# Kernel optimization log

Measured on AMD Instinct MI355X. Metric: run time of the kernel, lower is better.

## Reference

```python
import math
import jax, jax.numpy as jnp
import numpy as np
from jax import lax

B, T, C = 2, 4096, 2048
N_HEAD, N_KV, D = 16, 4, 128
WINDOW, DILATION, CHUNK = 256, 1, 128


def make_rope_cache(seq_len, n_elem, base=10000.0):
    theta = 1.0 / base ** (jnp.arange(0, n_elem, 2, dtype=jnp.float32) / n_elem)
    idx_theta = jnp.arange(seq_len, dtype=jnp.float32)[:, None] * theta[None, :]
    return jnp.stack([jnp.cos(idx_theta), jnp.sin(idx_theta)], axis=-1)  # [T, n_elem/2, 2]


def setup_inputs() -> dict:
    key = jax.random.key(0)
    ks = jax.random.split(key, 5)
    s = 1.0 / math.sqrt(C)
    return {
        "x": jax.random.normal(ks[0], (B, T, C), dtype=jnp.float32),
        "wq": jax.random.normal(ks[1], (N_HEAD * D, C), dtype=jnp.float32) * s,
        "wk": jax.random.normal(ks[2], (N_KV * D, C), dtype=jnp.float32) * s,
        "wv": jax.random.normal(ks[3], (N_KV * D, C), dtype=jnp.float32) * s,
        "wo": jax.random.normal(ks[4], (N_HEAD * D, C), dtype=jnp.float32).T * s,  # stored [out,in]
        "rope_cache": make_rope_cache(T, D),
    }


def apply_rope(xh, cache):
    # xh: [B, T, H, D]; cache: [T, D/2, 2]
    b, t, h, d = xh.shape
    xr = xh.reshape(b, t, h, d // 2, 2)
    cos = cache[:t, :, 0][None, :, None, :]
    sin = cache[:t, :, 1][None, :, None, :]
    x0, x1 = xr[..., 0], xr[..., 1]
    rot = jnp.stack([x0 * cos - x1 * sin, x0 * sin + x1 * cos], axis=-1)
    return rot.reshape(b, t, h, d)


def sliding_attention(q, k, v, window, dilation, chunk):
    # q,k,v: [B, H, T, D] -> [B, H, T, D]; O(T*window), memory bounded via scan over chunks
    b, h, t, d = q.shape
    w = min(window, (t + dilation - 1) // dilation)
    offsets = jnp.arange(w) * dilation
    scale = 1.0 / math.sqrt(d)
    n_chunks = t // chunk

    def step(carry, c):
        pos = c * chunk + jnp.arange(chunk)                       # [L]
        idx_raw = (pos - (w - 1) * dilation)[:, None] + offsets[None, :]  # [L, w]
        invalid = idx_raw < 0
        idx = jnp.clip(idx_raw, 0, t - 1)
        flat = idx.reshape(-1)
        k_win = jnp.take(k, flat, axis=2).reshape(b, h, chunk, w, d)
        v_win = jnp.take(v, flat, axis=2).reshape(b, h, chunk, w, d)
        q_c = lax.dynamic_slice_in_dim(q, c * chunk, chunk, axis=2)
        scores = jnp.einsum('bhld,bhlwd->bhlw', q_c.astype(jnp.float32),
                            k_win.astype(jnp.float32)) * scale
        scores = jnp.where(invalid[None, None], -jnp.inf, scores)
        attn = jax.nn.softmax(scores, axis=-1)
        out_c = jnp.einsum('bhlw,bhlwd->bhld', attn, v_win.astype(jnp.float32))
        return carry, out_c.astype(q.dtype)

    _, outs = lax.scan(step, None, jnp.arange(n_chunks))  # [n_chunks, B, H, chunk, D]
    return outs.transpose(1, 2, 0, 3, 4).reshape(b, h, t, d)


def reference(x, wq, wk, wv, wo, rope_cache):
    b, t, c = x.shape
    q = (x @ wq.T).reshape(b, t, N_HEAD, D)
    k = (x @ wk.T).reshape(b, t, N_KV, D)
    v = (x @ wv.T).reshape(b, t, N_KV, D)
    q = apply_rope(q, rope_cache)
    k = apply_rope(k, rope_cache)
    q = q.transpose(0, 2, 1, 3)  # [B, H, T, D]
    k = k.transpose(0, 2, 1, 3)
    v = v.transpose(0, 2, 1, 3)
    g = N_HEAD // N_KV
    k = jnp.repeat(k, g, axis=1)
    v = jnp.repeat(v, g, axis=1)
    y = sliding_attention(q, k, v, WINDOW, DILATION, CHUNK)
    y = y.transpose(0, 2, 1, 3).reshape(b, t, c)
    return y @ wo.T
```

## Files before the change

### kernel.cpp

```cpp
#include <hip/hip_runtime.h>
#include <stdint.h>

typedef unsigned short u16;
typedef __attribute__((ext_vector_type(8))) short bf16x8;
typedef __attribute__((ext_vector_type(8))) unsigned short u16x8;
typedef __attribute__((ext_vector_type(4))) float f32x4;

#define B_  2
#define T_  4096
#define C_  2048
#define NH  16
#define NKV 4
#define HD  128

__device__ __forceinline__ u16 f2bf(float f) {
  union { float f; uint32_t u; } v; v.f = f;
  uint32_t u = v.u;
  u += 0x7fffu + ((u >> 16) & 1u);
  return (u16)(u >> 16);
}
__device__ __forceinline__ float bf2f(u16 h) {
  union { uint32_t u; float f; } v; v.u = ((uint32_t)h) << 16;
  return v.f;
}

__device__ __forceinline__ void gload_lds16(const u16* g, u16* l) {
  __builtin_amdgcn_global_load_lds(
      (const __attribute__((address_space(1))) void*)g,
      (__attribute__((address_space(3))) void*)l, 16, 0, 0);
}

__global__ void cvt_all(const float* __restrict__ x, const float* __restrict__ wq,
                        const float* __restrict__ wk, const float* __restrict__ wv,
                        const float* __restrict__ wo, u16* __restrict__ xb,
                        u16* __restrict__ wqkv, u16* __restrict__ wob) {
  long i = ((long)blockIdx.x * 256 + threadIdx.x) * 4;
  const float* src; u16* dst; long off;
  if (i < 16777216L)      { src = x;  dst = xb;              off = i; }
  else if (i < 20971520L) { src = wq; dst = wqkv;            off = i - 16777216L; }
  else if (i < 22020096L) { src = wk; dst = wqkv + 4194304L; off = i - 20971520L; }
  else if (i < 23068672L) { src = wv; dst = wqkv + 5242880L; off = i - 22020096L; }
  else                    { src = wo; dst = wob;             off = i - 23068672L; }
  float4 v = *(const float4*)(src + off);
  ushort4 o4;
  o4.x = f2bf(v.x); o4.y = f2bf(v.y); o4.z = f2bf(v.z); o4.w = f2bf(v.w);
  *(ushort4*)(dst + off) = o4;
}

__global__ void krearr(const u16* __restrict__ qkv, u16* __restrict__ K2) {
  int gid = blockIdx.x * 256 + threadIdx.x;
  int r = gid & 65535, bk = gid >> 16;
  int l16 = r & 15, q4 = (r >> 4) & 3, ks = (r >> 6) & 3, kb = r >> 8;
  int bb = bk >> 2, kv = bk & 3;
  const u16* src = qkv + ((long)(bb * T_ + kb * 16 + l16)) * 3072 + 2048 + kv * HD +
                   ks * 32 + q4 * 8;
  *(u16x8*)(K2 + (long)bk * 524288 + (long)r * 8) = *(const u16x8*)src;
}

__global__ __launch_bounds__(256) void vrearr2(const u16* __restrict__ qkv,
                                               u16* __restrict__ V2) {
  const int bid = blockIdx.x;
  const int bk = bid >> 5, kc = bid & 31;
  const int bb = bk >> 2, kv = bk & 3;
  const int t = threadIdx.x;
  __shared__ u16 L[128 * 136];
  {
    int key = t >> 1;
    int dh = (t & 1) * 64;
    const u16* src = qkv + ((long)(bb * T_ + kc * 128 + key)) * 3072 + 2560 + kv * HD + dh;
    u16* dst = L + key * 136 + dh;
#pragma unroll
    for (int u = 0; u < 8; u++)
      *(u16x8*)(dst + u * 8) = *(const u16x8*)(src + u * 8);
  }
  __syncthreads();
  u16* out = V2 + (long)bk * 524288 + (long)kc * 16384;
#pragma unroll
  for (int step = 0; step < 8; step++) {
    int o = step * 256 + t;
    int l16 = o & 15, q4 = (o >> 4) & 3, ks = (o >> 6) & 3, jd = (o >> 8) & 7;
    int keyb = ks * 32 + q4 * 8;
    int d = jd * 16 + l16;
    u16x8 v;
#pragma unroll
    for (int e = 0; e < 8; e++) v[e] = L[(keyb + e) * 136 + d];
    *(u16x8*)(out + (long)o * 8) = v;
  }
}

#define GBAR() __builtin_amdgcn_s_barrier()
#define LGKM0() do { asm volatile("s_waitcnt lgkmcnt(0)" ::: "memory"); \
                     __builtin_amdgcn_sched_barrier(0); } while (0)

template <int WRITE_BF16, int ROPE>
__global__ __launch_bounds__(512, 2) void gemm256(const u16* __restrict__ A,
                                                  const u16* __restrict__ Bw,
                                                  void* __restrict__ Cv,
                                                  const float* __restrict__ rope,
                                                  int M, int N, int K) {
  __shared__ __align__(16) u16 lds[65536];
  const int tid = threadIdx.x;
  const int lane = tid & 63;
  const int wave = tid >> 6;
  const int q4 = lane >> 4, l16 = lane & 15;
  const int wm = wave >> 2, wn = wave & 3;

  const int nwg = gridDim.x * gridDim.y;
  const int orig = blockIdx.y * gridDim.x + blockIdx.x;
  const int swz = (orig & 7) * (nwg >> 3) + (orig >> 3);
  const int bm = swz / gridDim.x, bn = swz % gridDim.x;
  const long m0 = (long)bm * 256, n0 = (long)bn * 256;

  const int srow = tid >> 2;
  const int slot = tid & 3;
  const int sx = (slot ^ ((srow >> 1) & 3)) * 8;
  const u16* Ag0 = A + (m0 + srow) * K + sx;
  const u16* Ag1 = A + (m0 + srow + 128) * K + sx;
  const u16* Bg0 = Bw + (n0 + srow) * K + sx;
  const u16* Bg1 = Bw + (n0 + srow + 128) * K + sx;
  u16* ldst = lds + tid * 8;

  const int nkt = K >> 6;

#define STAGE_A(bufi, kh, kt)                                  \
  do {                                                         \
    long ko = ((long)(kt) << 6) + ((kh) << 5);                 \
    u16* d = ldst + (bufi) * 32768 + (kh) * 8192;              \
    gload_lds16(Ag0 + ko, d);                                  \
    gload_lds16(Ag1 + ko, d + 4096);                           \
  } while (0)
#define STAGE_B(bufi, kh, kt)                                  \
  do {                                                         \
    long ko = ((long)(kt) << 6) + ((kh) << 5);                 \
    u16* d = ldst + (bufi) * 32768 + 16384 + (kh) * 8192;      \
    gload_lds16(Bg0 + ko, d);                                  \
    gload_lds16(Bg1 + ko, d + 4096);                           \
  } while (0)

  int offA[8], offB[4];
#pragma unroll
  for (int m = 0; m < 8; m++) {
    int r = wm * 128 + m * 16 + l16;
    offA[m] = r * 32 + ((q4 ^ ((r >> 1) & 3)) << 3);
  }
#pragma unroll
  for (int n = 0; n < 4; n++) {
    int r = wn * 64 + n * 16 + l16;
    offB[n] = 16384 + r * 32 + ((q4 ^ ((r >> 1) & 3)) << 3);
  }

  f32x4 acc[8][4] = {};

  STAGE_A(0, 0, 0); STAGE_B(0, 0, 0); STAGE_A(0, 1, 0); STAGE_B(0, 1, 0);
  if (nkt > 1) {
    STAGE_A(1, 0, 1); STAGE_B(1, 0, 1);
    asm volatile("s_waitcnt vmcnt(4)" ::: "memory");
  } else {
    asm volatile("s_waitcnt vmcnt(0)" ::: "memory");
  }
  GBAR();

  bf16x8 afX[4], afY[4], bvA[4], bvB[4];
  for (int kt = 0; kt < nkt; kt++) {
    const int bo = (kt & 1) * 32768;
#pragma unroll
    for (int m = 0; m < 4; m++) afX[m] = *(const bf16x8*)(lds + bo + offA[m]);
#pragma unroll
    for (int n = 0; n < 4; n++) bvA[n] = *(const bf16x8*)(lds + bo + offB[n]);
    if (kt + 1 < nkt) STAGE_A((kt + 1) & 1, 1, kt + 1);
    LGKM0();
#pragma unroll
    for (int m = 0; m < 4; m++) afY[m] = *(const bf16x8*)(lds + bo + offA[4 + m]);
    __builtin_amdgcn_s_setprio(1);
#pragma unroll
    for (int m = 0; m < 4; m++)
#pragma unroll
      for (int n = 0; n < 4; n++)
        acc[m][n] = __builtin_amdgcn_mfma_f32_16x16x32_bf16(afX[m], bvA[n], acc[m][n], 0, 0, 0);
    __builtin_amdgcn_s_setprio(0);
    if (kt + 1 < nkt) STAGE_B((kt + 1) & 1, 1, kt + 1);
    LGKM0();
#pragma unroll
    for (int m = 0; m < 4; m++) afX[m] = *(const bf16x8*)(lds + bo + 8192 + offA[m]);
#pragma unroll
    for (int n = 0; n < 4; n++) bvB[n] = *(const bf16x8*)(lds + bo + 8192 + offB[n]);
    __builtin_amdgcn_s_setprio(1);
#pragma unroll
    for (int m = 0; m < 4; m++)
#pragma unroll
      for (int n = 0; n < 4; n++)
        acc[4 + m][n] = __builtin_amdgcn_mfma_f32_16x16x32_bf16(afY[m], bvA[n], acc[4 + m][n], 0, 0, 0);
    __builtin_amdgcn_s_setprio(0);
    GBAR();
    if (kt + 2 < nkt) STAGE_A(kt & 1, 0, kt + 2);
    LGKM0();
#pragma unroll
    for (int m = 0; m < 4; m++) afY[m] = *(const bf16x8*)(lds + bo + 8192 + offA[4 + m]);
    __builtin_amdgcn_s_setprio(1);
#pragma unroll
    for (int m = 0; m < 4; m++)
#pragma unroll
      for (int n = 0; n < 4; n++)
        acc[m][n] = __builtin_amdgcn_mfma_f32_16x16x32_bf16(afX[m], bvB[n], acc[m][n], 0, 0, 0);
    __builtin_amdgcn_s_setprio(0);
    if (kt + 2 < nkt) STAGE_B(kt & 1, 0, kt + 2);
    LGKM0();
    __builtin_amdgcn_s_setprio(1);
#pragma unroll
    for (int m = 0; m < 4; m++)
#pragma unroll
      for (int n = 0; n < 4; n++)
        acc[4 + m][n] = __builtin_amdgcn_mfma_f32_16x16x32_bf16(afY[m], bvB[n], acc[4 + m][n], 0, 0, 0);
    __builtin_amdgcn_s_setprio(0);
    if (kt + 2 < nkt)
      asm volatile("s_waitcnt vmcnt(4)" ::: "memory");
    else
      asm volatile("s_waitcnt vmcnt(0)" ::: "memory");
    GBAR();
  }
#undef STAGE_A
#undef STAGE_B

  if (ROPE) {
    float* rl = (float*)lds;
    const int rrow = tid >> 1;
    const int rh = (tid & 1) * 64;
    const int rx = ((rrow >> 2) & 3) << 3;
    const float* rsrc = rope + ((long)((int)((m0 + rrow)) & (T_ - 1)) * 128 + rh);
    float* rdst = rl + rrow * 128;
#pragma unroll
    for (int v = 0; v < 16; v++) {
      int col = rh + v * 4;
      *(float4*)(rdst + (col ^ rx)) = *(const float4*)(rsrc + v * 4);
    }
    GBAR();
  }

  const long crow0 = m0 + wm * 128;
  const long ccol0 = n0 + wn * 64;
  const float* rl = (const float*)lds;
#pragma unroll
  for (int m = 0; m < 8; m++)
#pragma unroll
    for (int n = 0; n < 4; n++) {
      const int cfrag = (int)(ccol0 + n * 16);
#pragma unroll
      for (int r = 0; r < 4; r++) {
        long row = crow0 + m * 16 + q4 * 4 + r;
        float x = acc[m][n][r];
        if (ROPE && cfrag < 2560) {
          int row_local = wm * 128 + m * 16 + q4 * 4 + r;
          int cc = ((cfrag & 127) + l16) ^ (q4 << 3);
          float2 cs = *(const float2*)(rl + row_local * 128 + (cc & ~1));
          float px = __shfl_xor(x, 1, 64);
          float rot = ((l16 & 1) == 0) ? (x * cs.x - px * cs.y)
                                       : (px * cs.y + x * cs.x);
          if (cfrag < 2048) rot *= 0.1275174315f;
          x = rot;
        }
        if (WRITE_BF16)
          ((u16*)Cv)[row * (long)N + ccol0 + n * 16 + l16] = f2bf(x);
        else
          ((float*)Cv)[row * (long)N + ccol0 + n * 16 + l16] = x;
      }
    }
}

__global__ __launch_bounds__(256, 2) void attn_kernel(const u16* __restrict__ qkv,
                                                      const u16* __restrict__ K2,
                                                      const u16* __restrict__ V2,
                                                      u16* __restrict__ y) {
  const int lin = blockIdx.x + (int)gridDim.x * (blockIdx.y + (int)gridDim.y * blockIdx.z);
  const int swz = (lin & 7) * 128 + (lin >> 3);
  const int tc = swz & 31, h = (swz >> 5) & 15, b = swz >> 9;
  const int t0 = tc * 128;
  const int kvh = h >> 2;
  __shared__ u16 Pl[4 * 32 * 136];
  __shared__ __align__(16) u16 Vl[16384];
  const int tid = threadIdx.x, wave = tid >> 6, lane = tid & 63;
  const int q4 = lane >> 4, l16 = lane & 15;
  u16* Pw = Pl + wave * (32 * 136);

  bf16x8 qf[2][4];
#pragma unroll
  for (int i = 0; i < 2; i++)
#pragma unroll
    for (int ks = 0; ks < 4; ks++)
      qf[i][ks] = *(const bf16x8*)(qkv +
          ((long)(b * T_ + t0 + 32 * wave + 16 * i + l16)) * 3072 + h * HD + ks * 32 + q4 * 8);

  f32x4 O[2][8] = {};
  float l_i[2][4] = {};

  const u16* Kb = K2 + (long)(b * NKV + kvh) * 524288 + lane * 8;
  const u16* Vb = V2 + (long)(b * NKV + kvh) * 524288;

  int kstart = t0 - 256; if (kstart < 0) kstart = 0;
  for (int k0 = kstart; k0 <= t0; k0 += 128) {
    const u16* Kc = Kb + (long)(k0 >> 4) * 2048;
    const u16* Vc = Vb + (long)(k0 >> 7) * 16384;
#pragma unroll
    for (int i = 0; i < 8; i++)
      gload_lds16(Vc + i * 2048 + tid * 8, Vl + i * 2048 + tid * 8);
    const int dbase0 = t0 + 32 * wave + q4 * 4 - k0 - l16;
    bf16x8 kr[2][4];
#pragma unroll
    for (int ks = 0; ks < 4; ks++) kr[0][ks] = *(const bf16x8*)(Kc + ks * 512);
#pragma unroll
    for (int ks = 0; ks < 4; ks++) kr[1][ks] = *(const bf16x8*)(Kc + 2048 + ks * 512);
#pragma unroll
    for (int j = 0; j < 8; j++) {
      bf16x8 kf[4];
#pragma unroll
      for (int ks = 0; ks < 4; ks++) kf[ks] = kr[j & 1][ks];
      if (j + 2 < 8)
#pragma unroll
        for (int ks = 0; ks < 4; ks++)
          kr[j & 1][ks] = *(const bf16x8*)(Kc + (j + 2) * 2048 + ks * 512);
      f32x4 s0 = {}, s1 = {};
#pragma unroll
      for (int ks = 0; ks < 4; ks++) {
        s0 = __builtin_amdgcn_mfma_f32_16x16x32_bf16(qf[0][ks], kf[ks], s0, 0, 0, 0);
        s1 = __builtin_amdgcn_mfma_f32_16x16x32_bf16(qf[1][ks], kf[ks], s1, 0, 0, 0);
      }
#pragma unroll
      for (int r = 0; r < 4; r++) {
        int d0 = dbase0 + r - 16 * j;
        float p0 = __builtin_amdgcn_exp2f(s0[r]);
        p0 = ((unsigned)d0 <= 255u) ? p0 : 0.f;
        l_i[0][r] += p0;
        Pw[(q4 * 4 + r) * 136 + 16 * j + l16] = f2bf(p0);
        int d1 = d0 + 16;
        float p1 = __builtin_amdgcn_exp2f(s1[r]);
        p1 = ((unsigned)d1 <= 255u) ? p1 : 0.f;
        l_i[1][r] += p1;
        Pw[(16 + q4 * 4 + r) * 136 + 16 * j + l16] = f2bf(p1);
      }
    }
    asm volatile("s_waitcnt vmcnt(0)" ::: "memory");
    GBAR();
    bf16x8 vr[4];
#pragma unroll
    for (int p = 0; p < 4; p++)
      vr[p] = *(const bf16x8*)(Vl + (p * 4) * 512 + lane * 8);
#pragma unroll
    for (int ks = 0; ks < 4; ks++) {
      bf16x8 pf0 = *(const bf16x8*)(&Pw[l16 * 136 + ks * 32 + q4 * 8]);
      bf16x8 pf1 = *(const bf16x8*)(&Pw[(16 + l16) * 136 + ks * 32 + q4 * 8]);
#pragma unroll
      for (int jd = 0; jd < 8; jd++) {
        const int s = ks * 8 + jd;
        bf16x8 vf = vr[s & 3];
        if (s + 4 < 32) {
          const int sn = s + 4, ksn = sn >> 3, jdn = sn & 7;
          vr[sn & 3] = *(const bf16x8*)(Vl + (jdn * 4 + ksn) * 512 + lane * 8);
        }
        O[0][jd] = __builtin_amdgcn_mfma_f32_16x16x32_bf16(pf0, vf, O[0][jd], 0, 0, 0);
        O[1][jd] = __builtin_amdgcn_mfma_f32_16x16x32_bf16(pf1, vf, O[1][jd], 0, 0, 0);
      }
    }
    GBAR();
  }
#pragma unroll
  for (int d = 1; d < 16; d <<= 1)
#pragma unroll
    for (int i = 0; i < 2; i++)
#pragma unroll
      for (int r = 0; r < 4; r++)
        l_i[i][r] += __shfl_xor(l_i[i][r], d, 64);
#pragma unroll
  for (int i = 0; i < 2; i++)
#pragma unroll
    for (int r = 0; r < 4; r++) {
      float inv = 1.0f / l_i[i][r];
      long row = (long)(b * T_ + t0 + 32 * wave + 16 * i + q4 * 4 + r);
#pragma unroll
      for (int jd = 0; jd < 8; jd++)
        y[row * 2048 + h * HD + 16 * jd + l16] = f2bf(O[i][jd][r] * inv);
    }
}

extern "C" void kernel_launch(void* const* d_in, const int* in_sizes, int n_in,
                              void* d_out, int out_size, void* d_ws, size_t ws_size,
                              hipStream_t stream) {
  const float* x    = (const float*)d_in[0];
  const float* wq   = (const float*)d_in[1];
  const float* wk   = (const float*)d_in[2];
  const float* wv   = (const float*)d_in[3];
  const float* wo   = (const float*)d_in[4];
  const float* rope = (const float*)d_in[5];
  float* out = (float*)d_out;

  u16* xb   = (u16*)d_ws;
  u16* wqkv = xb + (long)8192 * 2048;
  u16* wob  = wqkv + (long)3072 * 2048;
  u16* qkv  = wob + (long)2048 * 2048;
  u16* V2   = qkv + (long)8192 * 3072;
  u16* K2   = wqkv;
  u16* yb   = xb;

  cvt_all<<<dim3(26624), dim3(256), 0, stream>>>(x, wq, wk, wv, wo, xb, wqkv, wob);

  gemm256<1, 1><<<dim3(3072 / 256, 8192 / 256), dim3(512), 0, stream>>>(
      xb, wqkv, (void*)qkv, rope, 8192, 3072, 2048);

  krearr<<<dim3(2048), dim3(256), 0, stream>>>(qkv, K2);
  vrearr2<<<dim3(256), dim3(256), 0, stream>>>(qkv, V2);

  attn_kernel<<<dim3(T_ / 128, NH, B_), dim3(256), 0, stream>>>(qkv, K2, V2, yb);

  gemm256<0, 0><<<dim3(2048 / 256, 8192 / 256), dim3(512), 0, stream>>>(
      yb, wob, (void*)out, (const float*)nullptr, 8192, 2048, 2048);
}
```

Baseline: 393.8 us.

## Enlarge attention tiles to 256 queries with LDS-staged K and live-chunk skipping

The attention kernel now runs 512-thread blocks covering 256 query rows, so each K/V chunk staged in LDS serves eight waves instead of four. K tiles are loaded into shared memory with the next one double-buffered behind the PV phase, and 32-key sub-chunks outside a wave's sliding window are skipped in both QK and PV. Separately, the RoPE cos/sin LDS swizzle in the GEMM epilogue is changed to a per-row XOR at float2 granularity to reduce bank conflicts. Costs include more LDS per block, extra barriers, and possibly lower occupancy.

Result: slower. 412.0 us (+4.6%).

```diff
diff --git a/kernel.cpp b/kernel.cpp
--- a/kernel.cpp
+++ b/kernel.cpp
@@ -225,13 +225,17 @@
     float* rl = (float*)lds;
     const int rrow = tid >> 1;
     const int rh = (tid & 1) * 64;
-    const int rx = ((rrow >> 2) & 3) << 3;
+    const int rx = (rrow & 15) << 1;
     const float* rsrc = rope + ((long)((int)((m0 + rrow)) & (T_ - 1)) * 128 + rh);
     float* rdst = rl + rrow * 128;
 #pragma unroll
     for (int v = 0; v < 16; v++) {
-      int col = rh + v * 4;
-      *(float4*)(rdst + (col ^ rx)) = *(const float4*)(rsrc + v * 4);
+      float4 t = *(const float4*)(rsrc + v * 4);
+      int c0 = rh + v * 4;
+      float2 lo; lo.x = t.x; lo.y = t.y;
+      float2 hi; hi.x = t.z; hi.y = t.w;
+      *(float2*)(rdst + (c0 ^ rx)) = lo;
+      *(float2*)(rdst + ((c0 + 2) ^ rx)) = hi;
     }
     GBAR();
   }
@@ -250,8 +254,9 @@
         float x = acc[m][n][r];
         if (ROPE && cfrag < 2560) {
           int row_local = wm * 128 + m * 16 + q4 * 4 + r;
-          int cc = ((cfrag & 127) + l16) ^ (q4 << 3);
-          float2 cs = *(const float2*)(rl + row_local * 128 + (cc & ~1));
+          int rxr = (row_local & 15) << 1;
+          int cc = (cfrag & 127) + l16;
+          float2 cs = *(const float2*)(rl + row_local * 128 + ((cc & ~1) ^ rxr));
           float px = __shfl_xor(x, 1, 64);
           float rot = ((l16 & 1) == 0) ? (x * cs.x - px * cs.y)
                                        : (px * cs.y + x * cs.x);
@@ -266,20 +271,22 @@
     }
 }
 
-__global__ __launch_bounds__(256, 2) void attn_kernel(const u16* __restrict__ qkv,
+__global__ __launch_bounds__(512, 2) void attn_kernel(const u16* __restrict__ qkv,
                                                       const u16* __restrict__ K2,
                                                       const u16* __restrict__ V2,
                                                       u16* __restrict__ y) {
   const int lin = blockIdx.x + (int)gridDim.x * (blockIdx.y + (int)gridDim.y * blockIdx.z);
-  const int swz = (lin & 7) * 128 + (lin >> 3);
-  const int tc = swz & 31, h = (swz >> 5) & 15, b = swz >> 9;
-  const int t0 = tc * 128;
+  const int swz = (lin & 7) * 64 + (lin >> 3);
+  const int tc = swz & 15, h = (swz >> 4) & 15, b = swz >> 8;
+  const int t0 = tc * 256;
   const int kvh = h >> 2;
-  __shared__ u16 Pl[4 * 32 * 136];
+  __shared__ __align__(16) u16 Kl[16384];
   __shared__ __align__(16) u16 Vl[16384];
+  __shared__ u16 Pl[8 * 32 * 136];
   const int tid = threadIdx.x, wave = tid >> 6, lane = tid & 63;
   const int q4 = lane >> 4, l16 = lane & 15;
   u16* Pw = Pl + wave * (32 * 136);
+  const int wq0 = t0 + 32 * wave;
 
   bf16x8 qf[2][4];
 #pragma unroll
@@ -287,74 +294,86 @@
 #pragma unroll
     for (int ks = 0; ks < 4; ks++)
       qf[i][ks] = *(const bf16x8*)(qkv +
-          ((long)(b * T_ + t0 + 32 * wave + 16 * i + l16)) * 3072 + h * HD + ks * 32 + q4 * 8);
+          ((long)(b * T_ + wq0 + 16 * i + l16)) * 3072 + h * HD + ks * 32 + q4 * 8);
 
   f32x4 O[2][8] = {};
   float l_i[2][4] = {};
 
-  const u16* Kb = K2 + (long)(b * NKV + kvh) * 524288 + lane * 8;
-  const u16* Vb = V2 + (long)(b * NKV + kvh) * 524288;
+  const u16* KB = K2 + (long)(b * NKV + kvh) * 524288;
+  const u16* VB = V2 + (long)(b * NKV + kvh) * 524288;
 
   int kstart = t0 - 256; if (kstart < 0) kstart = 0;
-  for (int k0 = kstart; k0 <= t0; k0 += 128) {
-    const u16* Kc = Kb + (long)(k0 >> 4) * 2048;
-    const u16* Vc = Vb + (long)(k0 >> 7) * 16384;
-#pragma unroll
-    for (int i = 0; i < 8; i++)
-      gload_lds16(Vc + i * 2048 + tid * 8, Vl + i * 2048 + tid * 8);
-    const int dbase0 = t0 + 32 * wave + q4 * 4 - k0 - l16;
-    bf16x8 kr[2][4];
-#pragma unroll
-    for (int ks = 0; ks < 4; ks++) kr[0][ks] = *(const bf16x8*)(Kc + ks * 512);
-#pragma unroll
-    for (int ks = 0; ks < 4; ks++) kr[1][ks] = *(const bf16x8*)(Kc + 2048 + ks * 512);
-#pragma unroll
-    for (int j = 0; j < 8; j++) {
-      bf16x8 kf[4];
-#pragma unroll
-      for (int ks = 0; ks < 4; ks++) kf[ks] = kr[j & 1][ks];
-      if (j + 2 < 8)
+  const int kend = t0 + 128;
+
+  {
+    const u16* Kg = KB + ((long)(kstart >> 4)) * 2048;
+#pragma unroll
+    for (int i = 0; i < 4; i++)
+      gload_lds16(Kg + i * 4096 + tid * 8, Kl + i * 4096 + tid * 8);
+  }
+
+  for (int k0 = kstart; k0 <= kend; k0 += 128) {
+    {
+      const u16* Vg = VB + ((long)(k0 >> 7)) * 16384;
+#pragma unroll
+      for (int i = 0; i < 4; i++)
+        gload_lds16(Vg + i * 4096 + tid * 8, Vl + i * 4096 + tid * 8);
+    }
+    asm volatile("s_waitcnt vmcnt(4)" ::: "memory");
+    GBAR();
+    const int dbase0 = wq0 + q4 * 4 - k0 - l16;
+#pragma unroll
+    for (int kc = 0; kc < 4; kc++) {
+      const bool live = (k0 + 32 * kc <= wq0 + 31) && (k0 + 32 * kc + 31 >= wq0 - 255);
+      if (!live) continue;
+#pragma unroll
+      for (int jh = 0; jh < 2; jh++) {
+        const int j = kc * 2 + jh;
+        bf16x8 kf[4];
 #pragma unroll
         for (int ks = 0; ks < 4; ks++)
-          kr[j & 1][ks] = *(const bf16x8*)(Kc + (j + 2) * 2048 + ks * 512);
-      f32x4 s0 = {}, s1 = {};
-#pragma unroll
-      for (int ks = 0; ks < 4; ks++) {
-        s0 = __builtin_amdgcn_mfma_f32_16x16x32_bf16(qf[0][ks], kf[ks], s0, 0, 0, 0);
-        s1 = __builtin_amdgcn_mfma_f32_16x16x32_bf16(qf[1][ks], kf[ks], s1, 0, 0, 0);
+          kf[ks] = *(const bf16x8*)(Kl + j * 2048 + ks * 512 + lane * 8);
+        f32x4 s0 = {}, s1 = {};
+#pragma unroll
+        for (int ks = 0; ks < 4; ks++) {
+          s0 = __builtin_amdgcn_mfma_f32_16x16x32_bf16(qf[0][ks], kf[ks], s0, 0, 0, 0);
+          s1 = __builtin_amdgcn_mfma_f32_16x16x32_bf16(qf[1][ks], kf[ks], s1, 0, 0, 0);
+        }
+#pragma unroll
+        for (int r = 0; r < 4; r++) {
+          int d0 = dbase0 + r - 16 * j;
+          float p0 = __builtin_amdgcn_exp2f(s0[r]);
+          p0 = ((unsigned)d0 <= 255u) ? p0 : 0.f;
+          l_i[0][r] += p0;
+          Pw[(q4 * 4 + r) * 136 + 16 * j + l16] = f2bf(p0);
+          int d1 = d0 + 16;
+          float p1 = __builtin_amdgcn_exp2f(s1[r]);
+          p1 = ((unsigned)d1 <= 255u) ? p1 : 0.f;
+          l_i[1][r] += p1;
+          Pw[(16 + q4 * 4 + r) * 136 + 16 * j + l16] = f2bf(p1);
+        }
       }
-#pragma unroll
-      for (int r = 0; r < 4; r++) {
-        int d0 = dbase0 + r - 16 * j;
-        float p0 = __builtin_amdgcn_exp2f(s0[r]);
-        p0 = ((unsigned)d0 <= 255u) ? p0 : 0.f;
-        l_i[0][r] += p0;
-        Pw[(q4 * 4 + r) * 136 + 16 * j + l16] = f2bf(p0);
-        int d1 = d0 + 16;
-        float p1 = __builtin_amdgcn_exp2f(s1[r]);
-        p1 = ((unsigned)d1 <= 255u) ? p1 : 0.f;
-        l_i[1][r] += p1;
-        Pw[(16 + q4 * 4 + r) * 136 + 16 * j + l16] = f2bf(p1);
-      }
-    }
-    asm volatile("s_waitcnt vmcnt(0)" ::: "memory");
-    GBAR();
-    bf16x8 vr[4];
-#pragma unroll
-    for (int p = 0; p < 4; p++)
-      vr[p] = *(const bf16x8*)(Vl + (p * 4) * 512 + lane * 8);
+    }
+    GBAR();
+    if (k0 + 128 <= kend) {
+      const u16* Kg = KB + ((long)((k0 + 128) >> 4)) * 2048;
+#pragma unroll
+      for (int i = 0; i < 4; i++)
+        gload_lds16(Kg + i * 4096 + tid * 8, Kl + i * 4096 + tid * 8);
+      asm volatile("s_waitcnt vmcnt(4)" ::: "memory");
+    } else {
+      asm volatile("s_waitcnt vmcnt(0)" ::: "memory");
+    }
+    GBAR();
 #pragma unroll
     for (int ks = 0; ks < 4; ks++) {
+      const bool live = (k0 + 32 * ks <= wq0 + 31) && (k0 + 32 * ks + 31 >= wq0 - 255);
+      if (!live) continue;
       bf16x8 pf0 = *(const bf16x8*)(&Pw[l16 * 136 + ks * 32 + q4 * 8]);
       bf16x8 pf1 = *(const bf16x8*)(&Pw[(16 + l16) * 136 + ks * 32 + q4 * 8]);
 #pragma unroll
       for (int jd = 0; jd < 8; jd++) {
-        const int s = ks * 8 + jd;
-        bf16x8 vf = vr[s & 3];
-        if (s + 4 < 32) {
-          const int sn = s + 4, ksn = sn >> 3, jdn = sn & 7;
-          vr[sn & 3] = *(const bf16x8*)(Vl + (jdn * 4 + ksn) * 512 + lane * 8);
-        }
+        bf16x8 vf = *(const bf16x8*)(Vl + (jd * 4 + ks) * 512 + lane * 8);
         O[0][jd] = __builtin_amdgcn_mfma_f32_16x16x32_bf16(pf0, vf, O[0][jd], 0, 0, 0);
         O[1][jd] = __builtin_amdgcn_mfma_f32_16x16x32_bf16(pf1, vf, O[1][jd], 0, 0, 0);
       }
@@ -373,7 +392,7 @@
 #pragma unroll
     for (int r = 0; r < 4; r++) {
       float inv = 1.0f / l_i[i][r];
-      long row = (long)(b * T_ + t0 + 32 * wave + 16 * i + q4 * 4 + r);
+      long row = (long)(b * T_ + wq0 + 16 * i + q4 * 4 + r);
 #pragma unroll
       for (int jd = 0; jd < 8; jd++)
         y[row * 2048 + h * HD + 16 * jd + l16] = f2bf(O[i][jd][r] * inv);
@@ -407,7 +426,7 @@
   krearr<<<dim3(2048), dim3(256), 0, stream>>>(qkv, K2);
   vrearr2<<<dim3(256), dim3(256), 0, stream>>>(qkv, V2);
 
-  attn_kernel<<<dim3(T_ / 128, NH, B_), dim3(256), 0, stream>>>(qkv, K2, V2, yb);
+  attn_kernel<<<dim3(T_ / 256, NH, B_), dim3(512), 0, stream>>>(qkv, K2, V2, yb);
 
   gemm256<0, 0><<<dim3(2048 / 256, 8192 / 256), dim3(512), 0, stream>>>(
       yb, wob, (void*)out, (const float*)nullptr, 8192, 2048, 2048);
```
